# Performance work log

Measured on AMD Instinct MI355X. Metric: run time of the kernel, lower is better.

Reference implementation:

```python
import jax, jax.numpy as jnp
from jax import lax
import numpy as np

B, CIN, L = 16, 512, 1024
COUT, K = 1024, 5          # conv out channels (GLU halves to 512), kernel size
DW = 512                    # word_feat == attn_channels == img_conv channels
HW = 196                    # 14*14 image feature locations


def setup_inputs() -> dict:
    key = jax.random.key(0)
    ks = jax.random.split(key, 8)
    s = 0.02
    return {
        "x": jax.random.normal(ks[0], (B, CIN, L), jnp.float32),
        "word_embed": jax.random.normal(ks[1], (B, L, DW), jnp.float32),
        "img_conv": jax.random.normal(ks[2], (B, DW, 14, 14), jnp.float32),
        "prev_attn": jnp.zeros((B, L, HW), jnp.float32),  # passed through, unused
        "conv_v": jax.random.normal(ks[3], (COUT, CIN, K), jnp.float32) * s,
        "conv_g": jnp.ones((COUT,), jnp.float32),
        "conv_b": jnp.zeros((COUT,), jnp.float32),
        "fc1_w": jax.random.normal(ks[4], (DW, DW), jnp.float32) * s,
        "fc1_b": jnp.zeros((DW,), jnp.float32),
        "fc2_w": jax.random.normal(ks[5], (DW, DW), jnp.float32) * s,
        "fc2_b": jnp.zeros((DW,), jnp.float32),
    }


def reference(x, word_embed, img_conv, prev_attn,
              conv_v, conv_g, conv_b, fc1_w, fc1_b, fc2_w, fc2_b):
    k = conv_v.shape[-1]
    # weight norm (PyTorch default dim=0): w = g * v / ||v||_{(in,k)}
    v_norm = jnp.sqrt(jnp.sum(conv_v * conv_v, axis=(1, 2), keepdims=True))
    w = (conv_g[:, None, None] / v_norm) * conv_v
    # Conv1d, padding=k-1 on both sides -> length L + k - 1 after ConvS2S trim
    y = lax.conv_general_dilated(x, w, window_strides=(1,),
                                 padding=[(k - 1, k - 1)],
                                 dimension_numbers=("NCH", "OIH", "NCH"))
    y = y + conv_b[None, :, None]
    # dropout is identity in eval mode
    a, b = jnp.split(y, 2, axis=1)          # GLU over channel dim
    h = a * jax.nn.sigmoid(b)
    h = h[:, :, : -(k - 1)]                  # [B, DW, L]
    identity_attn = h
    # attn_fc1 on [B, L, DW] then add word embeddings
    q = jnp.einsum("bcl,ac->bla", h, fc1_w) + fc1_b + word_embed  # [B, L, DW]
    feat = img_conv.reshape(img_conv.shape[0], img_conv.shape[1], -1)  # [B, DW, HW]
    score = jnp.einsum("bla,bap->blp", q, feat)   # [B, L, HW]
    attn = jax.nn.softmax(score, axis=-1)         # softmax over image locations
    ctx = jnp.einsum("blp,bap->bla", attn, feat)  # [B, L, DW]
    o = jnp.einsum("bla,ca->blc", ctx, fc2_w) + fc2_b
    out = o.transpose(0, 2, 1) + identity_attn
    # identity.shape == out.shape (input_feat == output_feat/2) -> no downsample
    out = out + x
    return (out, word_embed, img_conv, attn)
```

## Files before the change

kernel.cpp:

```cpp
#include <hip/hip_runtime.h>
#include <math.h>

#define NB   16
#define NCIN 512
#define NL   1024
#define NCOUT 1024
#define NK   5
#define NDW  512
#define NHW  196
#define NP   208
#define NPK  224

typedef unsigned short ushort_t;
typedef unsigned int uint_t;
typedef __attribute__((ext_vector_type(8))) short bf16x8;
typedef __attribute__((ext_vector_type(4))) float f32x4;

static __device__ __forceinline__ ushort_t f2bf(float f) {
  uint_t u = __builtin_bit_cast(uint_t, f);
  u += 0x7fff + ((u >> 16) & 1);
  return (ushort_t)(u >> 16);
}
static __device__ __forceinline__ float bf2f(ushort_t u) {
  uint_t v = ((uint_t)u) << 16;
  return __builtin_bit_cast(float, v);
}

__global__ __launch_bounds__(256) void wnorm_kernel(
    const float* __restrict__ v, const float* __restrict__ g,
    ushort_t* __restrict__ wperm) {
  const int o = blockIdx.x;
  const float* vr = v + (size_t)o * (NCIN * NK);
  float s = 0.f;
  for (int j = threadIdx.x; j < NCIN * NK; j += 256) {
    float t = vr[j];
    s += t * t;
  }
  for (int off = 32; off; off >>= 1) s += __shfl_down(s, off, 64);
  __shared__ float red[4];
  __shared__ float scale_s;
  const int wid = threadIdx.x >> 6;
  if ((threadIdx.x & 63) == 0) red[wid] = s;
  __syncthreads();
  if (threadIdx.x == 0) {
    float tot = red[0] + red[1] + red[2] + red[3];
    scale_s = g[o] / sqrtf(tot);
  }
  __syncthreads();
  const float scale = scale_s;
#pragma unroll
  for (int dk = 0; dk < NK; ++dk) {
    for (int ci = threadIdx.x; ci < NCIN; ci += 256) {
      wperm[((size_t)dk * NCOUT + o) * NCIN + ci] = f2bf(vr[ci * NK + dk] * scale);
    }
  }
}

__global__ __launch_bounds__(256) void xpose_kernel(
    const float* __restrict__ x, ushort_t* __restrict__ xT) {
  const int b = blockIdx.z;
  const int ci0 = blockIdx.y * 64;
  const int l0 = blockIdx.x * 64;
  const int tid = threadIdx.x;
  __shared__ float t[64][65];
  const float* xb = x + ((size_t)b * NCIN + ci0) * NL + l0;
#pragma unroll
  for (int r = 0; r < 4; ++r) {
    int row = r * 16 + (tid >> 4);
    int col = (tid & 15) * 4;
    float4 v = *(const float4*)&xb[(size_t)row * NL + col];
    t[row][col + 0] = v.x; t[row][col + 1] = v.y;
    t[row][col + 2] = v.z; t[row][col + 3] = v.w;
  }
  __syncthreads();
  ushort_t* xo = xT + ((size_t)b * NL + l0) * NCIN + ci0;
#pragma unroll
  for (int r = 0; r < 4; ++r) {
    int lrow = r * 16 + (tid >> 4);
    int cic = (tid & 15) * 4;
    ushort4 o4;
    o4.x = f2bf(t[cic + 0][lrow]);
    o4.y = f2bf(t[cic + 1][lrow]);
    o4.z = f2bf(t[cic + 2][lrow]);
    o4.w = f2bf(t[cic + 3][lrow]);
    *(ushort4*)&xo[(size_t)lrow * NCIN + cic] = o4;
  }
}

__global__ __launch_bounds__(256) void wcvt_kernel(
    const float* __restrict__ w1, const float* __restrict__ w2,
    ushort_t* __restrict__ w1bf, ushort_t* __restrict__ w2bf) {
  const int i = (blockIdx.x * 256 + threadIdx.x) * 4;
  {
    float4 v = *(const float4*)&w1[i];
    ushort4 o; o.x = f2bf(v.x); o.y = f2bf(v.y); o.z = f2bf(v.z); o.w = f2bf(v.w);
    *(ushort4*)&w1bf[i] = o;
  }
  {
    float4 v = *(const float4*)&w2[i];
    ushort4 o; o.x = f2bf(v.x); o.y = f2bf(v.y); o.z = f2bf(v.z); o.w = f2bf(v.w);
    *(ushort4*)&w2bf[i] = o;
  }
}

__global__ __launch_bounds__(256) void ftrans_kernel(
    const float* __restrict__ feat, ushort_t* __restrict__ fThi,
    ushort_t* __restrict__ fTlo, ushort_t* __restrict__ fbf) {
  const int b = blockIdx.y;
  const int a0 = blockIdx.x * 64;
  const int tid = threadIdx.x;
  __shared__ float t[64][200];

  const float* fb_ = feat + ((size_t)b * NDW + a0) * NHW;
#pragma unroll
  for (int pp = 0; pp < 16; ++pp) {
    int row = pp * 4 + (tid >> 6);
#pragma unroll
    for (int cc = 0; cc < 4; ++cc) {
      int col = cc * 64 + (tid & 63);
      if (col < NHW) t[row][col] = fb_[(size_t)row * NHW + col];
    }
  }
  __syncthreads();

  for (int pp = 0; pp < 13; ++pp) {
    int p = pp * 16 + (tid >> 4);
    int j = (tid & 15) * 4;
    ushort4 hi4, lo4;
#pragma unroll
    for (int k = 0; k < 4; ++k) {
      float v = (p < NHW) ? t[j + k][p] : 0.f;
      ushort_t h = f2bf(v);
      float lof = v - bf2f(h);
      ushort_t l = f2bf(lof);
      ((ushort_t*)&hi4)[k] = h;
      ((ushort_t*)&lo4)[k] = l;
    }
    size_t base = ((size_t)b * NP + p) * NDW + a0 + j;
    *(ushort4*)&fThi[base] = hi4;
    *(ushort4*)&fTlo[base] = lo4;
  }

#pragma unroll
  for (int cc = 0; cc < 4; ++cc) {
    int col = cc * 64 + (tid & 63);
    if (col < NPK) {
#pragma unroll
      for (int rr = 0; rr < 16; ++rr) {
        int al = rr * 4 + (tid >> 6);
        float v = (col < NHW) ? t[al][col] : 0.f;
        fbf[((size_t)b * NDW + a0 + al) * NPK + col] = f2bf(v);
      }
    }
  }
}

__global__ __launch_bounds__(256, 2) void conv_glu_mfma(
    const ushort_t* __restrict__ xT, const ushort_t* __restrict__ wperm,
    const float* __restrict__ conv_b, ushort_t* __restrict__ hbfT) {
  const int b  = blockIdx.z;
  const int c0 = blockIdx.y * 128;
  const int l0 = blockIdx.x * 128;
  const int tid = threadIdx.x;
  const int wid = tid >> 6;
  const int lane = tid & 63;
  const int wl = wid & 1;
  const int wc = wid >> 1;
  const int quad = lane >> 4;
  const int l16 = lane & 15;

  __shared__ ushort_t lx[128][72];
  __shared__ ushort_t lw[256][72];

  f32x4 accA[4][4], accB[4][4];
#pragma unroll
  for (int mt = 0; mt < 4; ++mt)
#pragma unroll
    for (int nt = 0; nt < 4; ++nt) {
      accA[mt][nt] = (f32x4){0.f, 0.f, 0.f, 0.f};
      accB[mt][nt] = (f32x4){0.f, 0.f, 0.f, 0.f};
    }

  const ushort_t* xTb = xT + (size_t)b * NL * NCIN;

  for (int dk = 0; dk < NK; ++dk) {
    const int lbase = l0 + dk - 4;
    const ushort_t* wpb = wperm + (size_t)dk * NCOUT * NCIN;
    for (int ci0 = 0; ci0 < NCIN; ci0 += 64) {
      __syncthreads();
#pragma unroll
      for (int it = 0; it < 4; ++it) {
        int t = tid + it * 256;
        int r = t >> 3, seg = t & 7;
        int gl = lbase + r;
        uint4 v = make_uint4(0u, 0u, 0u, 0u);
        if (gl >= 0)
          v = *(const uint4*)(xTb + (size_t)gl * NCIN + ci0 + seg * 8);
        *(uint4*)&lx[r][seg * 8] = v;
      }
#pragma unroll
      for (int it = 0; it < 8; ++it) {
        int t = tid + it * 256;
        int r = t >> 3, seg = t & 7;
        int co = (it < 4) ? (c0 + r) : (384 + c0 + r);
        uint4 v = *(const uint4*)(wpb + (size_t)co * NCIN + ci0 + seg * 8);
        *(uint4*)&lw[r][seg * 8] = v;
      }
      __syncthreads();
#pragma unroll
      for (int ks = 0; ks < 2; ++ks) {
        bf16x8 af[4];
#pragma unroll
        for (int mt = 0; mt < 4; ++mt)
          af[mt] = *(const bf16x8*)&lx[wl * 64 + mt * 16 + l16][ks * 32 + quad * 8];
#pragma unroll
        for (int nt = 0; nt < 4; ++nt) {
          bf16x8 bfa = *(const bf16x8*)&lw[wc * 64 + nt * 16 + l16][ks * 32 + quad * 8];
          bf16x8 bfb = *(const bf16x8*)&lw[128 + wc * 64 + nt * 16 + l16][ks * 32 + quad * 8];
#pragma unroll
          for (int mt = 0; mt < 4; ++mt) {
            accA[mt][nt] = __builtin_amdgcn_mfma_f32_16x16x32_bf16(af[mt], bfa, accA[mt][nt], 0, 0, 0);
            accB[mt][nt] = __builtin_amdgcn_mfma_f32_16x16x32_bf16(af[mt], bfb, accB[mt][nt], 0, 0, 0);
          }
        }
      }
    }
  }

#pragma unroll
  for (int nt = 0; nt < 4; ++nt) {
    const int co = c0 + wc * 64 + nt * 16 + l16;
    const float ba = conv_b[co];
    const float bb = conv_b[co + 512];
#pragma unroll
    for (int mt = 0; mt < 4; ++mt) {
      const int l = l0 + wl * 64 + mt * 16 + quad * 4;
      f32x4 a4 = accA[mt][nt];
      f32x4 b4 = accB[mt][nt];
#pragma unroll
      for (int r = 0; r < 4; ++r) {
        float aa = a4[r] + ba, bg = b4[r] + bb;
        float hv = aa * (1.f / (1.f + __expf(-bg)));
        hbfT[((size_t)b * NL + l + r) * NDW + co] = f2bf(hv);
      }
    }
  }
}

__global__ __launch_bounds__(256, 2) void fc1_mfma(
    const ushort_t* __restrict__ hbfT, const ushort_t* __restrict__ w1bf,
    const float* __restrict__ fb, const float* __restrict__ we,
    ushort_t* __restrict__ qhi, ushort_t* __restrict__ qlo) {
  const int b  = blockIdx.z;
  const int a0 = blockIdx.y * 128;
  const int l0 = blockIdx.x * 128;
  const int tid = threadIdx.x;
  const int wid = tid >> 6;
  const int lane = tid & 63;
  const int wl = wid & 1;
  const int wc = wid >> 1;
  const int quad = lane >> 4;
  const int l16 = lane & 15;

  __shared__ ushort_t la[128][72];
  __shared__ ushort_t lb[128][72];

  f32x4 acc[4][4];
#pragma unroll
  for (int mt = 0; mt < 4; ++mt)
#pragma unroll
    for (int nt = 0; nt < 4; ++nt) acc[mt][nt] = (f32x4){0.f, 0.f, 0.f, 0.f};

  const ushort_t* hb = hbfT + (size_t)b * NL * NDW;

  for (int c0 = 0; c0 < NDW; c0 += 64) {
    __syncthreads();
#pragma unroll
    for (int it = 0; it < 4; ++it) {
      int t = tid + it * 256;
      int r = t >> 3, seg = t & 7;
      *(uint4*)&la[r][seg * 8] = *(const uint4*)(hb + (size_t)(l0 + r) * NDW + c0 + seg * 8);
    }
#pragma unroll
    for (int it = 0; it < 4; ++it) {
      int t = tid + it * 256;
      int r = t >> 3, seg = t & 7;
      *(uint4*)&lb[r][seg * 8] = *(const uint4*)(w1bf + (size_t)(a0 + r) * NDW + c0 + seg * 8);
    }
    __syncthreads();
#pragma unroll
    for (int ks = 0; ks < 2; ++ks) {
      bf16x8 af[4];
#pragma unroll
      for (int mt = 0; mt < 4; ++mt)
        af[mt] = *(const bf16x8*)&la[wl * 64 + mt * 16 + l16][ks * 32 + quad * 8];
#pragma unroll
      for (int nt = 0; nt < 4; ++nt) {
        bf16x8 bf = *(const bf16x8*)&lb[wc * 64 + nt * 16 + l16][ks * 32 + quad * 8];
#pragma unroll
        for (int mt = 0; mt < 4; ++mt)
          acc[mt][nt] = __builtin_amdgcn_mfma_f32_16x16x32_bf16(af[mt], bf, acc[mt][nt], 0, 0, 0);
      }
    }
  }

#pragma unroll
  for (int nt = 0; nt < 4; ++nt) {
    const int a = a0 + wc * 64 + nt * 16 + l16;
    const float bias = fb[a];
#pragma unroll
    for (int mt = 0; mt < 4; ++mt) {
      const int l = l0 + wl * 64 + mt * 16 + quad * 4;
#pragma unroll
      for (int r = 0; r < 4; ++r) {
        size_t idx = ((size_t)b * NL + l + r) * NDW + a;
        float qv = acc[mt][nt][r] + bias + we[idx];
        ushort_t h = f2bf(qv);
        float lof = qv - bf2f(h);
        qhi[idx] = h;
        qlo[idx] = f2bf(lof);
      }
    }
  }
}

__global__ __launch_bounds__(256) void score_softmax(
    const ushort_t* __restrict__ qhi, const ushort_t* __restrict__ qlo,
    const ushort_t* __restrict__ fThi, const ushort_t* __restrict__ fTlo,
    float* __restrict__ out_attn) {
  const int b  = blockIdx.y;
  const int l0 = blockIdx.x * 64;
  const int tid = threadIdx.x;
  const int wid = tid >> 6;
  const int lane = tid & 63;
  const int quad = lane >> 4;
  const int l16 = lane & 15;

  __shared__ ushort_t qh[64][36], ql[64][36];
  __shared__ ushort_t fh[208][36], fl[208][36];

  f32x4 acc[13];
#pragma unroll
  for (int nt = 0; nt < 13; ++nt) acc[nt] = (f32x4){0.f, 0.f, 0.f, 0.f};

  for (int kc = 0; kc < 16; ++kc) {
    const int a0 = kc * 32;
    __syncthreads();
    {
      int r = tid >> 2, seg = tid & 3;
      size_t src = ((size_t)b * NL + l0 + r) * NDW + a0 + seg * 8;
      *(uint4*)&qh[r][seg * 8] = *(const uint4*)(qhi + src);
      *(uint4*)&ql[r][seg * 8] = *(const uint4*)(qlo + src);
#pragma unroll
      for (int it = 0; it < 4; ++it) {
        int row = it * 64 + (tid >> 2);
        if (row < NP) {
          size_t fsrc = ((size_t)b * NP + row) * NDW + a0 + seg * 8;
          *(uint4*)&fh[row][seg * 8] = *(const uint4*)(fThi + fsrc);
          *(uint4*)&fl[row][seg * 8] = *(const uint4*)(fTlo + fsrc);
        }
      }
    }
    __syncthreads();
    bf16x8 ah = *(const bf16x8*)&qh[wid * 16 + l16][quad * 8];
    bf16x8 al = *(const bf16x8*)&ql[wid * 16 + l16][quad * 8];
#pragma unroll
    for (int nt = 0; nt < 13; ++nt) {
      bf16x8 bh = *(const bf16x8*)&fh[nt * 16 + l16][quad * 8];
      bf16x8 bl = *(const bf16x8*)&fl[nt * 16 + l16][quad * 8];
      acc[nt] = __builtin_amdgcn_mfma_f32_16x16x32_bf16(ah, bh, acc[nt], 0, 0, 0);
      acc[nt] = __builtin_amdgcn_mfma_f32_16x16x32_bf16(al, bh, acc[nt], 0, 0, 0);
      acc[nt] = __builtin_amdgcn_mfma_f32_16x16x32_bf16(ah, bl, acc[nt], 0, 0, 0);
    }
  }

  const bool v12 = (l16 < 4);
#pragma unroll
  for (int r = 0; r < 4; ++r) {
    float mx = -1e30f;
#pragma unroll
    for (int nt = 0; nt < 12; ++nt) mx = fmaxf(mx, acc[nt][r]);
    if (v12) mx = fmaxf(mx, acc[12][r]);
#pragma unroll
    for (int off = 1; off < 16; off <<= 1) mx = fmaxf(mx, __shfl_xor(mx, off, 16));
    float ex[13];
    float sum = 0.f;
#pragma unroll
    for (int nt = 0; nt < 12; ++nt) { ex[nt] = __expf(acc[nt][r] - mx); sum += ex[nt]; }
    ex[12] = v12 ? __expf(acc[12][r] - mx) : 0.f;
    sum += ex[12];
#pragma unroll
    for (int off = 1; off < 16; off <<= 1) sum += __shfl_xor(sum, off, 16);
    const float inv = 1.f / sum;
    const int l = l0 + wid * 16 + quad * 4 + r;
    float* ao = out_attn + ((size_t)b * NL + l) * NHW;
#pragma unroll
    for (int nt = 0; nt < 13; ++nt) {
      int p = nt * 16 + l16;
      if (p < NHW) ao[p] = ex[nt] * inv;
    }
  }
}

__global__ __launch_bounds__(256, 2) void ctx_mfma(
    const float* __restrict__ attn, const ushort_t* __restrict__ fbf,
    ushort_t* __restrict__ ctx_bf) {
  const int b  = blockIdx.z;
  const int a0 = blockIdx.y * 128;
  const int l0 = blockIdx.x * 128;
  const int tid = threadIdx.x;
  const int wid = tid >> 6;
  const int lane = tid & 63;
  const int wl = wid & 1;
  const int wc = wid >> 1;
  const int quad = lane >> 4;
  const int l16 = lane & 15;

  __shared__ ushort_t la[128][36];
  __shared__ ushort_t lb[128][36];

  f32x4 acc[4][4];
#pragma unroll
  for (int mt = 0; mt < 4; ++mt)
#pragma unroll
    for (int nt = 0; nt < 4; ++nt) acc[mt][nt] = (f32x4){0.f, 0.f, 0.f, 0.f};

  for (int kc = 0; kc < 7; ++kc) {
    const int p0 = kc * 32;
    __syncthreads();
#pragma unroll
    for (int it = 0; it < 2; ++it) {
      int r = it * 64 + (tid >> 2), seg = tid & 3;
      int pb = p0 + seg * 8;
      const float* src = attn + ((size_t)b * NL + l0 + r) * NHW + pb;
      ushort4 o[2];
      if (pb + 7 < NHW) {
        float4 v0 = *(const float4*)src;
        float4 v1 = *(const float4*)(src + 4);
        o[0].x = f2bf(v0.x); o[0].y = f2bf(v0.y); o[0].z = f2bf(v0.z); o[0].w = f2bf(v0.w);
        o[1].x = f2bf(v1.x); o[1].y = f2bf(v1.y); o[1].z = f2bf(v1.z); o[1].w = f2bf(v1.w);
      } else {
#pragma unroll
        for (int k = 0; k < 8; ++k) {
          float v = (pb + k < NHW) ? src[k] : 0.f;
          ((ushort_t*)o)[k] = f2bf(v);
        }
      }
      *(uint4*)&la[r][seg * 8] = *(uint4*)o;
      const ushort_t* fsrc = fbf + ((size_t)b * NDW + a0 + r) * NPK + pb;
      *(uint4*)&lb[r][seg * 8] = *(const uint4*)fsrc;
    }
    __syncthreads();
    bf16x8 af[4];
#pragma unroll
    for (int mt = 0; mt < 4; ++mt)
      af[mt] = *(const bf16x8*)&la[wl * 64 + mt * 16 + l16][quad * 8];
#pragma unroll
    for (int nt = 0; nt < 4; ++nt) {
      bf16x8 bf = *(const bf16x8*)&lb[wc * 64 + nt * 16 + l16][quad * 8];
#pragma unroll
      for (int mt = 0; mt < 4; ++mt)
        acc[mt][nt] = __builtin_amdgcn_mfma_f32_16x16x32_bf16(af[mt], bf, acc[mt][nt], 0, 0, 0);
    }
  }

#pragma unroll
  for (int nt = 0; nt < 4; ++nt) {
    const int a = a0 + wc * 64 + nt * 16 + l16;
#pragma unroll
    for (int mt = 0; mt < 4; ++mt) {
      const int l = l0 + wl * 64 + mt * 16 + quad * 4;
#pragma unroll
      for (int r = 0; r < 4; ++r)
        ctx_bf[((size_t)b * NL + l + r) * NDW + a] = f2bf(acc[mt][nt][r]);
    }
  }
}

__global__ __launch_bounds__(256, 2) void fc2_mfma(
    const ushort_t* __restrict__ w2bf, const ushort_t* __restrict__ ctx_bf,
    const float* __restrict__ fb2, const ushort_t* __restrict__ hbfT,
    const float* __restrict__ x, float* __restrict__ out0) {
  const int b  = blockIdx.z;
  const int c0 = blockIdx.y * 128;
  const int l0 = blockIdx.x * 128;
  const int tid = threadIdx.x;
  const int wid = tid >> 6;
  const int lane = tid & 63;
  const int wl = wid & 1;
  const int wc = wid >> 1;
  const int quad = lane >> 4;
  const int l16 = lane & 15;

  __shared__ ushort_t la[128][72];
  __shared__ ushort_t lb[128][72];

  f32x4 acc[4][4];
#pragma unroll
  for (int mt = 0; mt < 4; ++mt)
#pragma unroll
    for (int nt = 0; nt < 4; ++nt) acc[mt][nt] = (f32x4){0.f, 0.f, 0.f, 0.f};

  for (int a0 = 0; a0 < NDW; a0 += 64) {
    __syncthreads();
#pragma unroll
    for (int it = 0; it < 4; ++it) {
      int t = tid + it * 256;
      int r = t >> 3, seg = t & 7;
      *(uint4*)&la[r][seg * 8] = *(const uint4*)(w2bf + (size_t)(c0 + r) * NDW + a0 + seg * 8);
    }
#pragma unroll
    for (int it = 0; it < 4; ++it) {
      int t = tid + it * 256;
      int r = t >> 3, seg = t & 7;
      *(uint4*)&lb[r][seg * 8] =
          *(const uint4*)(ctx_bf + ((size_t)b * NL + l0 + r) * NDW + a0 + seg * 8);
    }
    __syncthreads();
#pragma unroll
    for (int ks = 0; ks < 2; ++ks) {
      bf16x8 af[4];
#pragma unroll
      for (int mt = 0; mt < 4; ++mt)
        af[mt] = *(const bf16x8*)&la[wl * 64 + mt * 16 + l16][ks * 32 + quad * 8];
#pragma unroll
      for (int nt = 0; nt < 4; ++nt) {
        bf16x8 bf = *(const bf16x8*)&lb[wc * 64 + nt * 16 + l16][ks * 32 + quad * 8];
#pragma unroll
        for (int mt = 0; mt < 4; ++mt)
          acc[mt][nt] = __builtin_amdgcn_mfma_f32_16x16x32_bf16(af[mt], bf, acc[mt][nt], 0, 0, 0);
      }
    }
  }

#pragma unroll
  for (int mt = 0; mt < 4; ++mt) {
    const int cb = c0 + wl * 64 + mt * 16 + quad * 4;
    float4 bias4 = *(const float4*)&fb2[cb];
#pragma unroll
    for (int nt = 0; nt < 4; ++nt) {
      const int l = l0 + wc * 64 + nt * 16 + l16;
      ushort4 h4 = *(const ushort4*)&hbfT[((size_t)b * NL + l) * NDW + cb];
      const float bias[4] = {bias4.x, bias4.y, bias4.z, bias4.w};
      const ushort_t hs[4] = {h4.x, h4.y, h4.z, h4.w};
#pragma unroll
      for (int r = 0; r < 4; ++r) {
        size_t idx = ((size_t)b * NDW + cb + r) * NL + l;
        out0[idx] = acc[mt][nt][r] + bias[r] + bf2f(hs[r]) + x[idx];
      }
    }
  }
}

extern "C" void kernel_launch(void* const* d_in, const int* in_sizes, int n_in,
                              void* d_out, int out_size, void* d_ws, size_t ws_size,
                              hipStream_t stream) {
  const float* x      = (const float*)d_in[0];
  const float* we     = (const float*)d_in[1];
  const float* img    = (const float*)d_in[2];
  const float* conv_v = (const float*)d_in[4];
  const float* conv_g = (const float*)d_in[5];
  const float* conv_b = (const float*)d_in[6];
  const float* fc1_w  = (const float*)d_in[7];
  const float* fc1_b  = (const float*)d_in[8];
  const float* fc2_w  = (const float*)d_in[9];
  const float* fc2_b  = (const float*)d_in[10];

  float* out0     = (float*)d_out;
  float* out_we   = out0 + 8388608;
  float* out_img  = out_we + 8388608;
  float* out_attn = out_img + 1605632;

  ushort_t* wsu = (ushort_t*)d_ws;
  ushort_t* qhi   = wsu;
  ushort_t* qlo   = wsu + 8388608;
  ushort_t* wperm = wsu;
  ushort_t* xT    = wsu + 2621440;
  ushort_t* ctx_b = wsu;
  ushort_t* hbfT  = wsu + 16777216;
  ushort_t* w1bf  = wsu + 25165824;
  ushort_t* w2bf  = wsu + 25428968 - 263144 + 262144 + 144;
  w2bf = wsu + 25165824 + 262144;
  ushort_t* fThi  = wsu + 25690112;
  ushort_t* fTlo  = wsu + 27394048;
  ushort_t* fbf   = wsu + 29097984;

  wnorm_kernel<<<dim3(NCOUT), 256, 0, stream>>>(conv_v, conv_g, wperm);
  xpose_kernel<<<dim3(16, 8, NB), 256, 0, stream>>>(x, xT);
  wcvt_kernel<<<dim3(256), 256, 0, stream>>>(fc1_w, fc2_w, w1bf, w2bf);
  ftrans_kernel<<<dim3(8, NB), 256, 0, stream>>>(img, fThi, fTlo, fbf);

  conv_glu_mfma<<<dim3(8, 4, NB), 256, 0, stream>>>(xT, wperm, conv_b, hbfT);
  fc1_mfma<<<dim3(8, 4, NB), 256, 0, stream>>>(hbfT, w1bf, fc1_b, we, qhi, qlo);
  score_softmax<<<dim3(16, NB), 256, 0, stream>>>(qhi, qlo, fThi, fTlo, out_attn);
  ctx_mfma<<<dim3(8, 4, NB), 256, 0, stream>>>(out_attn, fbf, ctx_b);
  fc2_mfma<<<dim3(8, 4, NB), 256, 0, stream>>>(w2bf, ctx_b, fc2_b, hbfT, x, out0);

  hipMemcpyAsync(out_we, we, (size_t)8388608 * sizeof(float),
                 hipMemcpyDeviceToDevice, stream);
  hipMemcpyAsync(out_img, img, (size_t)1605632 * sizeof(float),
                 hipMemcpyDeviceToDevice, stream);
}
```

Baseline: 430.0 us.

## Fuse score, softmax and context into one kernel; fold passthrough copies into kernels

Merges score_softmax and ctx_mfma into a single attn_fused kernel. It keeps the normalized attention tile in LDS as bf16 and multiplies it directly against the image features, so the fp32 attention no longer has to be re-read from global memory. The score loop now register-prefetches the next feature chunk and splits the 64×208 score tile across 4 waves, with a cross-wave reduction through shared memory for the softmax. The word_embed and img_conv passthrough copies become extra stores inside fc1 and ftrans, removing the two device-to-device memcpys. In exchange, attn_fused runs only 256 blocks, each looping over 8 feature chunks, so parallelism is low and LDS use is high.

After: 458.1 us. 6.5% more time.

```diff
diff --git a/kernel.cpp b/kernel.cpp
--- a/kernel.cpp
+++ b/kernel.cpp
@@ -105,7 +105,8 @@
 
 __global__ __launch_bounds__(256) void ftrans_kernel(
     const float* __restrict__ feat, ushort_t* __restrict__ fThi,
-    ushort_t* __restrict__ fTlo, ushort_t* __restrict__ fbf) {
+    ushort_t* __restrict__ fTlo, ushort_t* __restrict__ fbf,
+    float* __restrict__ out_img) {
   const int b = blockIdx.y;
   const int a0 = blockIdx.x * 64;
   const int tid = threadIdx.x;
@@ -118,7 +119,11 @@
 #pragma unroll
     for (int cc = 0; cc < 4; ++cc) {
       int col = cc * 64 + (tid & 63);
-      if (col < NHW) t[row][col] = fb_[(size_t)row * NHW + col];
+      if (col < NHW) {
+        float v = fb_[(size_t)row * NHW + col];
+        t[row][col] = v;
+        out_img[((size_t)b * NDW + a0 + row) * NHW + col] = v;
+      }
     }
   }
   __syncthreads();
@@ -250,7 +255,8 @@
 __global__ __launch_bounds__(256, 2) void fc1_mfma(
     const ushort_t* __restrict__ hbfT, const ushort_t* __restrict__ w1bf,
     const float* __restrict__ fb, const float* __restrict__ we,
-    ushort_t* __restrict__ qhi, ushort_t* __restrict__ qlo) {
+    ushort_t* __restrict__ qhi, ushort_t* __restrict__ qlo,
+    float* __restrict__ out_we) {
   const int b  = blockIdx.z;
   const int a0 = blockIdx.y * 128;
   const int l0 = blockIdx.x * 128;
@@ -314,7 +320,9 @@
 #pragma unroll
       for (int r = 0; r < 4; ++r) {
         size_t idx = ((size_t)b * NL + l + r) * NDW + a;
-        float qv = acc[mt][nt][r] + bias + we[idx];
+        float wev = we[idx];
+        out_we[idx] = wev;
+        float qv = acc[mt][nt][r] + bias + wev;
         ushort_t h = f2bf(qv);
         float lof = qv - bf2f(h);
         qhi[idx] = h;
@@ -324,10 +332,11 @@
   }
 }
 
-__global__ __launch_bounds__(256) void score_softmax(
+__global__ __launch_bounds__(256) void attn_fused(
     const ushort_t* __restrict__ qhi, const ushort_t* __restrict__ qlo,
     const ushort_t* __restrict__ fThi, const ushort_t* __restrict__ fTlo,
-    float* __restrict__ out_attn) {
+    const ushort_t* __restrict__ fbf,
+    float* __restrict__ out_attn, ushort_t* __restrict__ ctx_bf) {
   const int b  = blockIdx.y;
   const int l0 = blockIdx.x * 64;
   const int tid = threadIdx.x;
@@ -335,145 +344,191 @@
   const int lane = tid & 63;
   const int quad = lane >> 4;
   const int l16 = lane & 15;
-
-  __shared__ ushort_t qh[64][36], ql[64][36];
-  __shared__ ushort_t fh[208][36], fl[208][36];
-
-  f32x4 acc[13];
-#pragma unroll
-  for (int nt = 0; nt < 13; ++nt) acc[nt] = (f32x4){0.f, 0.f, 0.f, 0.f};
+  const int wm = wid & 1;
+  const int wn = wid >> 1;
+
+  __shared__ ushort_t smem[31488];
+  ushort_t* fh  = smem;
+  ushort_t* fl  = smem + 8320;
+  ushort_t* as_ = smem;
+  ushort_t* fbt = smem + 16640;
+  __shared__ float rmx[64][2];
+  __shared__ float rsm[64][2];
+
+  const int NT = wn ? 6 : 7;
+  const int ntbase = wn ? 7 : 0;
+
+  f32x4 acc[2][7];
+#pragma unroll
+  for (int mt = 0; mt < 2; ++mt)
+#pragma unroll
+    for (int nt = 0; nt < 7; ++nt) acc[mt][nt] = (f32x4){0.f, 0.f, 0.f, 0.f};
+
+  const int frow = tid >> 2;
+  const int fseg = (tid & 3) * 8;
+
+  uint4 pfh[4], pfl[4];
+#pragma unroll
+  for (int it = 0; it < 4; ++it) {
+    int r = it * 64 + frow;
+    if (r < NP) {
+      size_t src = ((size_t)b * NP + r) * NDW + fseg;
+      pfh[it] = *(const uint4*)(fThi + src);
+      pfl[it] = *(const uint4*)(fTlo + src);
+    }
+  }
 
   for (int kc = 0; kc < 16; ++kc) {
-    const int a0 = kc * 32;
-    __syncthreads();
-    {
-      int r = tid >> 2, seg = tid & 3;
-      size_t src = ((size_t)b * NL + l0 + r) * NDW + a0 + seg * 8;
-      *(uint4*)&qh[r][seg * 8] = *(const uint4*)(qhi + src);
-      *(uint4*)&ql[r][seg * 8] = *(const uint4*)(qlo + src);
+    __syncthreads();
+#pragma unroll
+    for (int it = 0; it < 4; ++it) {
+      int r = it * 64 + frow;
+      if (r < NP) {
+        *(uint4*)&fh[r * 40 + fseg] = pfh[it];
+        *(uint4*)&fl[r * 40 + fseg] = pfl[it];
+      }
+    }
+    __syncthreads();
+    if (kc < 15) {
 #pragma unroll
       for (int it = 0; it < 4; ++it) {
-        int row = it * 64 + (tid >> 2);
-        if (row < NP) {
-          size_t fsrc = ((size_t)b * NP + row) * NDW + a0 + seg * 8;
-          *(uint4*)&fh[row][seg * 8] = *(const uint4*)(fThi + fsrc);
-          *(uint4*)&fl[row][seg * 8] = *(const uint4*)(fTlo + fsrc);
+        int r = it * 64 + frow;
+        if (r < NP) {
+          size_t src = ((size_t)b * NP + r) * NDW + (kc + 1) * 32 + fseg;
+          pfh[it] = *(const uint4*)(fThi + src);
+          pfl[it] = *(const uint4*)(fTlo + src);
         }
       }
     }
-    __syncthreads();
-    bf16x8 ah = *(const bf16x8*)&qh[wid * 16 + l16][quad * 8];
-    bf16x8 al = *(const bf16x8*)&ql[wid * 16 + l16][quad * 8];
-#pragma unroll
-    for (int nt = 0; nt < 13; ++nt) {
-      bf16x8 bh = *(const bf16x8*)&fh[nt * 16 + l16][quad * 8];
-      bf16x8 bl = *(const bf16x8*)&fl[nt * 16 + l16][quad * 8];
-      acc[nt] = __builtin_amdgcn_mfma_f32_16x16x32_bf16(ah, bh, acc[nt], 0, 0, 0);
-      acc[nt] = __builtin_amdgcn_mfma_f32_16x16x32_bf16(al, bh, acc[nt], 0, 0, 0);
-      acc[nt] = __builtin_amdgcn_mfma_f32_16x16x32_bf16(ah, bl, acc[nt], 0, 0, 0);
-    }
-  }
-
-  const bool v12 = (l16 < 4);
-#pragma unroll
-  for (int r = 0; r < 4; ++r) {
-    float mx = -1e30f;
-#pragma unroll
-    for (int nt = 0; nt < 12; ++nt) mx = fmaxf(mx, acc[nt][r]);
-    if (v12) mx = fmaxf(mx, acc[12][r]);
-#pragma unroll
-    for (int off = 1; off < 16; off <<= 1) mx = fmaxf(mx, __shfl_xor(mx, off, 16));
-    float ex[13];
-    float sum = 0.f;
-#pragma unroll
-    for (int nt = 0; nt < 12; ++nt) { ex[nt] = __expf(acc[nt][r] - mx); sum += ex[nt]; }
-    ex[12] = v12 ? __expf(acc[12][r] - mx) : 0.f;
-    sum += ex[12];
-#pragma unroll
-    for (int off = 1; off < 16; off <<= 1) sum += __shfl_xor(sum, off, 16);
-    const float inv = 1.f / sum;
-    const int l = l0 + wid * 16 + quad * 4 + r;
-    float* ao = out_attn + ((size_t)b * NL + l) * NHW;
-#pragma unroll
-    for (int nt = 0; nt < 13; ++nt) {
-      int p = nt * 16 + l16;
-      if (p < NHW) ao[p] = ex[nt] * inv;
-    }
-  }
-}
-
-__global__ __launch_bounds__(256, 2) void ctx_mfma(
-    const float* __restrict__ attn, const ushort_t* __restrict__ fbf,
-    ushort_t* __restrict__ ctx_bf) {
-  const int b  = blockIdx.z;
-  const int a0 = blockIdx.y * 128;
-  const int l0 = blockIdx.x * 128;
-  const int tid = threadIdx.x;
-  const int wid = tid >> 6;
-  const int lane = tid & 63;
-  const int wl = wid & 1;
-  const int wc = wid >> 1;
-  const int quad = lane >> 4;
-  const int l16 = lane & 15;
-
-  __shared__ ushort_t la[128][36];
-  __shared__ ushort_t lb[128][36];
-
-  f32x4 acc[4][4];
-#pragma unroll
-  for (int mt = 0; mt < 4; ++mt)
-#pragma unroll
-    for (int nt = 0; nt < 4; ++nt) acc[mt][nt] = (f32x4){0.f, 0.f, 0.f, 0.f};
-
-  for (int kc = 0; kc < 7; ++kc) {
-    const int p0 = kc * 32;
-    __syncthreads();
-#pragma unroll
-    for (int it = 0; it < 2; ++it) {
-      int r = it * 64 + (tid >> 2), seg = tid & 3;
-      int pb = p0 + seg * 8;
-      const float* src = attn + ((size_t)b * NL + l0 + r) * NHW + pb;
-      ushort4 o[2];
-      if (pb + 7 < NHW) {
-        float4 v0 = *(const float4*)src;
-        float4 v1 = *(const float4*)(src + 4);
-        o[0].x = f2bf(v0.x); o[0].y = f2bf(v0.y); o[0].z = f2bf(v0.z); o[0].w = f2bf(v0.w);
-        o[1].x = f2bf(v1.x); o[1].y = f2bf(v1.y); o[1].z = f2bf(v1.z); o[1].w = f2bf(v1.w);
-      } else {
-#pragma unroll
-        for (int k = 0; k < 8; ++k) {
-          float v = (pb + k < NHW) ? src[k] : 0.f;
-          ((ushort_t*)o)[k] = f2bf(v);
+    bf16x8 ah[2], alo[2];
+#pragma unroll
+    for (int mt = 0; mt < 2; ++mt) {
+      int lq = l0 + wm * 32 + mt * 16 + l16;
+      size_t base = ((size_t)b * NL + lq) * NDW + kc * 32 + quad * 8;
+      ah[mt]  = *(const bf16x8*)(qhi + base);
+      alo[mt] = *(const bf16x8*)(qlo + base);
+    }
+#pragma unroll
+    for (int ntl = 0; ntl < 7; ++ntl) {
+      if (ntl >= NT) break;
+      int ntg = ntbase + ntl;
+      bf16x8 bh = *(const bf16x8*)&fh[(ntg * 16 + l16) * 40 + quad * 8];
+      bf16x8 bl = *(const bf16x8*)&fl[(ntg * 16 + l16) * 40 + quad * 8];
+#pragma unroll
+      for (int mt = 0; mt < 2; ++mt) {
+        acc[mt][ntl] = __builtin_amdgcn_mfma_f32_16x16x32_bf16(ah[mt],  bh, acc[mt][ntl], 0, 0, 0);
+        acc[mt][ntl] = __builtin_amdgcn_mfma_f32_16x16x32_bf16(alo[mt], bh, acc[mt][ntl], 0, 0, 0);
+        acc[mt][ntl] = __builtin_amdgcn_mfma_f32_16x16x32_bf16(ah[mt],  bl, acc[mt][ntl], 0, 0, 0);
+      }
+    }
+  }
+
+#pragma unroll
+  for (int mt = 0; mt < 2; ++mt)
+#pragma unroll
+    for (int r = 0; r < 4; ++r) {
+      float m = -3e38f;
+#pragma unroll
+      for (int ntl = 0; ntl < 7; ++ntl) {
+        if (ntl >= NT) break;
+        bool valid = !(wn == 1 && ntl == 5 && l16 >= 4);
+        if (valid) m = fmaxf(m, acc[mt][ntl][r]);
+      }
+#pragma unroll
+      for (int off = 1; off < 16; off <<= 1) m = fmaxf(m, __shfl_xor(m, off, 16));
+      if (l16 == 0) rmx[wm * 32 + mt * 16 + quad * 4 + r][wn] = m;
+    }
+  __syncthreads();
+  float inv_[2][4];
+#pragma unroll
+  for (int mt = 0; mt < 2; ++mt)
+#pragma unroll
+    for (int r = 0; r < 4; ++r) {
+      int row = wm * 32 + mt * 16 + quad * 4 + r;
+      float g = fmaxf(rmx[row][0], rmx[row][1]);
+      float s = 0.f;
+#pragma unroll
+      for (int ntl = 0; ntl < 7; ++ntl) {
+        if (ntl >= NT) break;
+        bool valid = !(wn == 1 && ntl == 5 && l16 >= 4);
+        float e = valid ? __expf(acc[mt][ntl][r] - g) : 0.f;
+        acc[mt][ntl][r] = e;
+        s += e;
+      }
+#pragma unroll
+      for (int off = 1; off < 16; off <<= 1) s += __shfl_xor(s, off, 16);
+      if (l16 == 0) rsm[row][wn] = s;
+    }
+  __syncthreads();
+#pragma unroll
+  for (int mt = 0; mt < 2; ++mt)
+#pragma unroll
+    for (int r = 0; r < 4; ++r) {
+      int row = wm * 32 + mt * 16 + quad * 4 + r;
+      float inv = 1.f / (rsm[row][0] + rsm[row][1]);
+      inv_[mt][r] = inv;
+      float* ao = out_attn + ((size_t)b * NL + l0 + row) * NHW;
+#pragma unroll
+      for (int ntl = 0; ntl < 7; ++ntl) {
+        if (ntl >= NT) break;
+        int p = (ntbase + ntl) * 16 + l16;
+        float vv = acc[mt][ntl][r] * inv;
+        as_[row * 232 + p] = f2bf(vv);
+        if (p < NHW) ao[p] = vv;
+      }
+    }
+  (void)inv_;
+  {
+    int row = tid >> 2;
+    int col = 208 + (tid & 3) * 4;
+    ushort4 z4; z4.x = 0; z4.y = 0; z4.z = 0; z4.w = 0;
+    *(ushort4*)&as_[row * 232 + col] = z4;
+  }
+  __syncthreads();
+
+  bf16x8 af[2][7];
+#pragma unroll
+  for (int mt = 0; mt < 2; ++mt)
+#pragma unroll
+    for (int kc = 0; kc < 7; ++kc)
+      af[mt][kc] = *(const bf16x8*)&as_[(wm * 32 + mt * 16 + l16) * 232 + kc * 32 + quad * 8];
+
+  for (int ac = 0; ac < 8; ++ac) {
+    const int ac0 = ac * 64;
+    __syncthreads();
+#pragma unroll
+    for (int it = 0; it < 7; ++it) {
+      int sg = it * 4 + (tid & 3);
+      *(uint4*)&fbt[frow * 232 + sg * 8] =
+          *(const uint4*)(fbf + ((size_t)b * NDW + ac0 + frow) * NPK + sg * 8);
+    }
+    __syncthreads();
+    f32x4 c2[2][2];
+#pragma unroll
+    for (int mt = 0; mt < 2; ++mt)
+#pragma unroll
+      for (int j2 = 0; j2 < 2; ++j2) c2[mt][j2] = (f32x4){0.f, 0.f, 0.f, 0.f};
+#pragma unroll
+    for (int kc = 0; kc < 7; ++kc) {
+      bf16x8 bf0 = *(const bf16x8*)&fbt[((wn * 2 + 0) * 16 + l16) * 232 + kc * 32 + quad * 8];
+      bf16x8 bf1 = *(const bf16x8*)&fbt[((wn * 2 + 1) * 16 + l16) * 232 + kc * 32 + quad * 8];
+#pragma unroll
+      for (int mt = 0; mt < 2; ++mt) {
+        c2[mt][0] = __builtin_amdgcn_mfma_f32_16x16x32_bf16(af[mt][kc], bf0, c2[mt][0], 0, 0, 0);
+        c2[mt][1] = __builtin_amdgcn_mfma_f32_16x16x32_bf16(af[mt][kc], bf1, c2[mt][1], 0, 0, 0);
+      }
+    }
+#pragma unroll
+    for (int mt = 0; mt < 2; ++mt)
+#pragma unroll
+      for (int j2 = 0; j2 < 2; ++j2) {
+        int a = ac0 + (wn * 2 + j2) * 16 + l16;
+#pragma unroll
+        for (int r = 0; r < 4; ++r) {
+          int l = l0 + wm * 32 + mt * 16 + quad * 4 + r;
+          ctx_bf[((size_t)b * NL + l) * NDW + a] = f2bf(c2[mt][j2][r]);
         }
       }
-      *(uint4*)&la[r][seg * 8] = *(uint4*)o;
-      const ushort_t* fsrc = fbf + ((size_t)b * NDW + a0 + r) * NPK + pb;
-      *(uint4*)&lb[r][seg * 8] = *(const uint4*)fsrc;
-    }
-    __syncthreads();
-    bf16x8 af[4];
-#pragma unroll
-    for (int mt = 0; mt < 4; ++mt)
-      af[mt] = *(const bf16x8*)&la[wl * 64 + mt * 16 + l16][quad * 8];
-#pragma unroll
-    for (int nt = 0; nt < 4; ++nt) {
-      bf16x8 bf = *(const bf16x8*)&lb[wc * 64 + nt * 16 + l16][quad * 8];
-#pragma unroll
-      for (int mt = 0; mt < 4; ++mt)
-        acc[mt][nt] = __builtin_amdgcn_mfma_f32_16x16x32_bf16(af[mt], bf, acc[mt][nt], 0, 0, 0);
-    }
-  }
-
-#pragma unroll
-  for (int nt = 0; nt < 4; ++nt) {
-    const int a = a0 + wc * 64 + nt * 16 + l16;
-#pragma unroll
-    for (int mt = 0; mt < 4; ++mt) {
-      const int l = l0 + wl * 64 + mt * 16 + quad * 4;
-#pragma unroll
-      for (int r = 0; r < 4; ++r)
-        ctx_bf[((size_t)b * NL + l + r) * NDW + a] = f2bf(acc[mt][nt][r]);
-    }
   }
 }
 
@@ -579,8 +634,7 @@
   ushort_t* ctx_b = wsu;
   ushort_t* hbfT  = wsu + 16777216;
   ushort_t* w1bf  = wsu + 25165824;
-  ushort_t* w2bf  = wsu + 25428968 - 263144 + 262144 + 144;
-  w2bf = wsu + 25165824 + 262144;
+  ushort_t* w2bf  = wsu + 25165824 + 262144;
   ushort_t* fThi  = wsu + 25690112;
   ushort_t* fTlo  = wsu + 27394048;
   ushort_t* fbf   = wsu + 29097984;
@@ -588,16 +642,11 @@
   wnorm_kernel<<<dim3(NCOUT), 256, 0, stream>>>(conv_v, conv_g, wperm);
   xpose_kernel<<<dim3(16, 8, NB), 256, 0, stream>>>(x, xT);
   wcvt_kernel<<<dim3(256), 256, 0, stream>>>(fc1_w, fc2_w, w1bf, w2bf);
-  ftrans_kernel<<<dim3(8, NB), 256, 0, stream>>>(img, fThi, fTlo, fbf);
+  ftrans_kernel<<<dim3(8, NB), 256, 0, stream>>>(img, fThi, fTlo, fbf, out_img);
 
   conv_glu_mfma<<<dim3(8, 4, NB), 256, 0, stream>>>(xT, wperm, conv_b, hbfT);
-  fc1_mfma<<<dim3(8, 4, NB), 256, 0, stream>>>(hbfT, w1bf, fc1_b, we, qhi, qlo);
-  score_softmax<<<dim3(16, NB), 256, 0, stream>>>(qhi, qlo, fThi, fTlo, out_attn);
-  ctx_mfma<<<dim3(8, 4, NB), 256, 0, stream>>>(out_attn, fbf, ctx_b);
+  fc1_mfma<<<dim3(8, 4, NB), 256, 0, stream>>>(hbfT, w1bf, fc1_b, we, qhi, qlo, out_we);
+  attn_fused<<<dim3(16, NB), 256, 0, stream>>>(qhi, qlo, fThi, fTlo, fbf,
+                                               out_attn, ctx_b);
   fc2_mfma<<<dim3(8, 4, NB), 256, 0, stream>>>(w2bf, ctx_b, fc2_b, hbfT, x, out0);
-
-  hipMemcpyAsync(out_we, we, (size_t)8388608 * sizeof(float),
-                 hipMemcpyDeviceToDevice, stream);
-  hipMemcpyAsync(out_img, img, (size_t)1605632 * sizeof(float),
-                 hipMemcpyDeviceToDevice, stream);
-}
+}
```
